# Performance work log

Measured on AMD Instinct MI355X. Metric: run time of the kernel, lower is better.

Reference implementation:

```python
import jax, jax.numpy as jnp
import numpy as np

B, L, H, NE, SPAN = 16, 2048, 768, 64, 4
EPS_COS = 1e-8   # torch cosine_similarity eps
EPS_STD = 1e-5   # std stabilizer from the module


def _linear_init(key, fan_in, fan_out):
    s = 1.0 / np.sqrt(fan_in)
    kw, kb = jax.random.split(key)
    w = jax.random.uniform(kw, (fan_in, fan_out), jnp.float32, -s, s)
    b = jax.random.uniform(kb, (fan_out,), jnp.float32, -s, s)
    return w, b


def setup_inputs() -> dict:
    key = jax.random.key(0)
    ks = jax.random.split(key, 6)
    w1, b1 = _linear_init(ks[0], 2 * H + 1, H)
    w2, b2 = _linear_init(ks[1], H, 512)
    w3, b3 = _linear_init(ks[2], 512, 256)
    w4, b4 = _linear_init(ks[3], 256, 2)
    x = jax.random.normal(ks[4], (B, L, H), jnp.float32)
    entity_starts = jax.random.randint(ks[5], (B, NE), 0, L - SPAN)
    threshold = jnp.float32(0.9)
    return dict(x=x, threshold=threshold,
                w1=w1, b1=b1, w2=w2, b2=b2, w3=w3, b3=b3, w4=w4, b4=b4,
                entity_starts=entity_starts)


def reference(x, threshold, w1, b1, w2, b2, w3, b3, w4, b4, entity_starts):
    # --- per-entity span max-pool (segment-max over x) ---
    # gather span tokens: [B, NE*SPAN] token indices into the L axis
    idx = (entity_starts[:, :, None] + jnp.arange(SPAN)).reshape(B, NE * SPAN)
    spans = jnp.take_along_axis(x, idx[:, :, None], axis=1)      # [B, NE*SPAN, H]
    emb = spans.reshape(B, NE, SPAN, H).max(axis=2)               # [B, NE, H]

    # --- pairwise cosine similarity per batch ---
    norm = jnp.maximum(jnp.linalg.norm(emb, axis=-1, keepdims=True), EPS_COS)
    n = emb / norm
    cos = jnp.einsum('bie,bje->bij', n, n)                        # [B, NE, NE]
    std = jnp.std(cos, axis=(1, 2), ddof=1, keepdims=True)        # torch .std() is unbiased
    sim = (cos - threshold) / (std + EPS_STD)
    sim = jnp.triu(sim, k=1)

    # --- all i<j pairs: [sim, emb_i, emb_j] ---
    iu, ju = np.triu_indices(NE, k=1)                             # static pair indices
    feats = jnp.concatenate(
        [sim[:, iu, ju, None], emb[:, iu, :], emb[:, ju, :]], axis=-1
    ).reshape(-1, 2 * H + 1)                                      # [B*P, 2H+1]

    # --- classifier MLP (dropout = identity at eval) ---
    h = jax.nn.relu(feats @ w1 + b1)
    h = jax.nn.relu(h @ w2 + b2)
    h = jax.nn.relu(h @ w3 + b3)
    logits = h @ w4 + b4                                          # [B*P, 2]
    return logits
```

## Files before the change

### kernel.cpp

```cpp
#include <hip/hip_runtime.h>
#include <cstdint>
#include <cstddef>

#define B_    16
#define L_    2048
#define H_    768
#define NE_   64
#define SPAN_ 4
#define NPAIR 2016
#define NROWS (B_ * NPAIR)

typedef __bf16 bf16_t;
typedef __bf16 bf16x8 __attribute__((ext_vector_type(8)));
typedef __bf16 bf16x4 __attribute__((ext_vector_type(4)));
typedef float  floatx4 __attribute__((ext_vector_type(4)));

#define OFF_EMBH   ((size_t)3145728)
#define OFF_N      ((size_t)4718592)
#define OFF_COS    ((size_t)7864320)
#define OFF_SIM    ((size_t)8126464)
#define OFF_W1ABT  ((size_t)8255488)
#define OFF_W2T    ((size_t)10614784)
#define OFF_W3T    ((size_t)11401216)
#define OFF_C1     ((size_t)11663360)
#define OFF_H2     ((size_t)67500032)
#define OFF_FLAG   ((size_t)117045248)
#define OFF_CANON  ((size_t)117045504)

__device__ int compute_flag(const unsigned short* __restrict__ xu) {
  __shared__ int tot[4];
  int t = threadIdx.x;
  int bad = 0;
  for (int i = t; i < 4096; i += 256) {
    int e = (xu[i] >> 7) & 0xFF;
    if (e > 133 || (e > 0 && e < 90)) bad++;
  }
  for (int off = 32; off > 0; off >>= 1) bad += __shfl_down(bad, off, 64);
  if ((t & 63) == 0) tot[t >> 6] = bad;
  __syncthreads();
  int f = ((tot[0] + tot[1] + tot[2] + tot[3]) > 200) ? 1 : 0;
  __syncthreads();
  return f;
}

__device__ inline bf16_t cvt_elem(const void* p, size_t i, int isf) {
  if (isf) return (bf16_t)(((const float*)p)[i]);
  return ((const bf16_t*)p)[i];
}

__global__ __launch_bounds__(256) void prep_kernel(
    const unsigned short* __restrict__ xu,
    const void* __restrict__ w1, const void* __restrict__ w2,
    const void* __restrict__ w3, const void* __restrict__ b1,
    const void* __restrict__ b2, const void* __restrict__ b3,
    const void* __restrict__ w4, const void* __restrict__ b4,
    int* __restrict__ flagout,
    bf16_t* __restrict__ w1abT, bf16_t* __restrict__ w2T,
    bf16_t* __restrict__ w3T, bf16_t* __restrict__ canon) {
  int blk = blockIdx.x;
  int t = threadIdx.x;
  int isf = compute_flag(xu);
  if (blk == 1664) {
    if (t == 0) flagout[0] = isf;
    for (int idx = t; idx < 2818; idx += 256) {
      if (idx < 768)       canon[idx] = cvt_elem(w1, idx, isf);
      else if (idx < 1536) canon[idx] = cvt_elem(b1, idx - 768, isf);
      else if (idx < 2048) canon[idx] = cvt_elem(b2, idx - 1536, isf);
      else if (idx < 2304) canon[idx] = cvt_elem(b3, idx - 2048, isf);
      else if (idx < 2816) canon[idx] = cvt_elem(w4, idx - 2304, isf);
      else                 canon[idx] = cvt_elem(b4, idx - 2816, isf);
    }
    return;
  }
  const void* src; size_t srcoff; bf16_t* dst; int K, N; int tix;
  if (blk < 576)       { src = w1; srcoff = 768;               dst = w1abT;          K = 768; N = 768; tix = blk; }
  else if (blk < 1152) { src = w1; srcoff = (size_t)769 * 768; dst = w1abT + 589824; K = 768; N = 768; tix = blk - 576; }
  else if (blk < 1536) { src = w2; srcoff = 0;                 dst = w2T;            K = 768; N = 512; tix = blk - 1152; }
  else                 { src = w3; srcoff = 0;                 dst = w3T;            K = 512; N = 256; tix = blk - 1536; }
  int tiles_k = K >> 5;
  int tn_t = tix / tiles_k, tk_t = tix - tn_t * tiles_k;
  __shared__ bf16_t tile[32][33];
  int ty = t >> 5, tx = t & 31;
#pragma unroll
  for (int p = 0; p < 4; p++) {
    int kk = tk_t * 32 + p * 8 + ty;
    int nn = tn_t * 32 + tx;
    tile[p * 8 + ty][tx] = cvt_elem(src, srcoff + (size_t)kk * N + nn, isf);
  }
  __syncthreads();
#pragma unroll
  for (int p = 0; p < 4; p++) {
    int nn = tn_t * 32 + p * 8 + ty;
    int kk = tk_t * 32 + tx;
    dst[(size_t)nn * K + kk] = tile[tx][p * 8 + ty];
  }
}

__global__ __launch_bounds__(1024) void embsim_kernel(
    const void* __restrict__ xv, const int* __restrict__ starts,
    const int* __restrict__ flagp, const void* __restrict__ thr_ptr,
    bf16_t* __restrict__ embh, float* __restrict__ simv) {
  __shared__ __align__(16) bf16_t nrm[64 * 768];
  __shared__ float red1[16], red2[16];
  __shared__ float scale_s, thr_s;
  int b = blockIdx.x;
  int t = threadIdx.x;
  int isf = flagp[0];

  int e   = t >> 4;
  int l16 = t & 15;
  int d0  = l16 * 48;
  int st  = starts[b * NE_ + e];
  size_t off = ((size_t)(b * L_ + st)) * H_;
  float ss = 0.f;
  bf16x8 pv[6];
  if (isf) {
    const float* xp = (const float*)xv + off + d0;
    for (int c8 = 0; c8 < 6; c8++) {
      const float* p = xp + c8 * 8;
      bf16x8 o;
#pragma unroll
      for (int h = 0; h < 2; h++) {
        floatx4 r0 = *(const floatx4*)(p + h * 4);
        floatx4 r1 = *(const floatx4*)(p + H_ + h * 4);
        floatx4 r2 = *(const floatx4*)(p + 2 * H_ + h * 4);
        floatx4 r3 = *(const floatx4*)(p + 3 * H_ + h * 4);
#pragma unroll
        for (int q = 0; q < 4; q++) {
          float v = fmaxf(fmaxf(r0[q], r1[q]), fmaxf(r2[q], r3[q]));
          ss += v * v;
          o[h * 4 + q] = (bf16_t)v;
        }
      }
      pv[c8] = o;
    }
  } else {
    const bf16_t* xp = (const bf16_t*)xv + off + d0;
    for (int c8 = 0; c8 < 6; c8++) {
      const bf16_t* p = xp + c8 * 8;
      bf16x8 r0 = *(const bf16x8*)(p);
      bf16x8 r1 = *(const bf16x8*)(p + H_);
      bf16x8 r2 = *(const bf16x8*)(p + 2 * H_);
      bf16x8 r3 = *(const bf16x8*)(p + 3 * H_);
      bf16x8 o;
#pragma unroll
      for (int q = 0; q < 8; q++) {
        float v = fmaxf(fmaxf((float)r0[q], (float)r1[q]),
                        fmaxf((float)r2[q], (float)r3[q]));
        ss += v * v;
        o[q] = (bf16_t)v;
      }
      pv[c8] = o;
    }
  }
#pragma unroll
  for (int d = 1; d < 16; d <<= 1) ss += __shfl_xor(ss, d, 64);
  float inv = 1.0f / fmaxf(sqrtf(ss), 1e-8f);

  size_t gb = ((size_t)(b * 64 + e)) * 768 + d0;
  int rowbyte = e * 1536;
  int xw = (e & 7) << 4;
  for (int c8 = 0; c8 < 6; c8++) {
    *(bf16x8*)(embh + gb + c8 * 8) = pv[c8];
    bf16x8 o;
#pragma unroll
    for (int q = 0; q < 8; q++) o[q] = (bf16_t)((float)pv[c8][q] * inv);
    int byo = (rowbyte + (d0 + c8 * 8) * 2) ^ xw;
    *(bf16x8*)((char*)nrm + byo) = o;
  }
  __syncthreads();

  int w = t >> 6, lane = t & 63;
  int quad = lane >> 4, l15 = lane & 15;
  int ti = w >> 2, tj = w & 3;
  int rowA = ti * 16 + l15, rowB = tj * 16 + l15;
  int xa = (rowA & 7) << 4, xb = (rowB & 7) << 4;
  const char* nb = (const char*)nrm;
  floatx4 acc = {};
#pragma unroll 4
  for (int k0 = 0; k0 < 768; k0 += 32) {
    int cb = (k0 + quad * 8) * 2;
    bf16x8 aF = *(const bf16x8*)(nb + ((rowA * 1536 + cb) ^ xa));
    bf16x8 bF = *(const bf16x8*)(nb + ((rowB * 1536 + cb) ^ xb));
    acc = __builtin_amdgcn_mfma_f32_16x16x32_bf16(aF, bF, acc, 0, 0, 0);
  }

  float s1 = acc[0] + acc[1] + acc[2] + acc[3];
  float s2 = acc[0] * acc[0] + acc[1] * acc[1] + acc[2] * acc[2] + acc[3] * acc[3];
#pragma unroll
  for (int d = 32; d > 0; d >>= 1) {
    s1 += __shfl_xor(s1, d, 64);
    s2 += __shfl_xor(s2, d, 64);
  }
  if (lane == 0) { red1[w] = s1; red2[w] = s2; }
  __syncthreads();
  if (t == 0) {
    float S1 = 0.f, S2 = 0.f;
#pragma unroll
    for (int i = 0; i < 16; i++) { S1 += red1[i]; S2 += red2[i]; }
    float mean = S1 * (1.0f / 4096.0f);
    float var = (S2 - 4096.0f * mean * mean) * (1.0f / 4095.0f);
    float sd = sqrtf(fmaxf(var, 0.f));
    scale_s = 1.0f / (sd + 1e-5f);
    thr_s = isf ? *(const float*)thr_ptr : (float)(*(const bf16_t*)thr_ptr);
  }
  __syncthreads();
  float sc = scale_s, th = thr_s;
  int ibase = ti * 16 + quad * 4;
  int j = tj * 16 + l15;
#pragma unroll
  for (int r = 0; r < 4; r++) {
    int i = ibase + r;
    if (j > i) {
      int p = i * 63 - (i * (i - 1)) / 2 + (j - i - 1);
      simv[b * NPAIR + p] = (acc[r] - th) * sc;
    }
  }
}

__global__ __launch_bounds__(256) void gemm1_kernel(
    const bf16_t* __restrict__ A, const bf16_t* __restrict__ Bt,
    float* __restrict__ C) {
  const int K = 768, N = 1536;
  __shared__ __align__(16) bf16_t Asm[64 * 32];
  __shared__ __align__(16) bf16_t Bsm[128 * 32];
  int bm = blockIdx.x, bn = blockIdx.y;
  int t = threadIdx.x;
  int w = t >> 6, lane = t & 63;
  int quad = lane >> 4, l15 = lane & 15;
  int wm = w >> 1, wn = w & 1;

  floatx4 acc[2][4] = {};
  const char* Abase = (const char*)(A + (size_t)bm * 64 * K);
  const char* Bbase = (const char*)(Bt + (size_t)bn * 128 * K);
  const int rowbytes = K * 2;

  for (int k0 = 0; k0 < K; k0 += 32) {
    {
      int fo = w * 1024 + lane * 16;
      int row = fo >> 6, colb = fo & 63;
      __builtin_amdgcn_global_load_lds(
          (__attribute__((address_space(1))) char*)(Abase + (size_t)row * rowbytes + k0 * 2 + colb),
          (__attribute__((address_space(3))) char*)((char*)Asm + w * 1024),
          16, 0, 0);
    }
#pragma unroll
    for (int it = 0; it < 2; it++) {
      int fo = (w * 2 + it) * 1024 + lane * 16;
      int row = fo >> 6, colb = fo & 63;
      __builtin_amdgcn_global_load_lds(
          (__attribute__((address_space(1))) char*)(Bbase + (size_t)row * rowbytes + k0 * 2 + colb),
          (__attribute__((address_space(3))) char*)((char*)Bsm + (w * 2 + it) * 1024),
          16, 0, 0);
    }
    __syncthreads();

    bf16x8 aF[2], bF[4];
#pragma unroll
    for (int tm = 0; tm < 2; tm++)
      aF[tm] = *((const bf16x8*)(Asm + (wm * 32 + tm * 16 + l15) * 32 + quad * 8));
#pragma unroll
    for (int tn = 0; tn < 4; tn++)
      bF[tn] = *((const bf16x8*)(Bsm + (wn * 64 + tn * 16 + l15) * 32 + quad * 8));
#pragma unroll
    for (int tm = 0; tm < 2; tm++)
#pragma unroll
      for (int tn = 0; tn < 4; tn++)
        acc[tm][tn] = __builtin_amdgcn_mfma_f32_16x16x32_bf16(aF[tm], bF[tn], acc[tm][tn], 0, 0, 0);
    __syncthreads();
  }

#pragma unroll
  for (int tm = 0; tm < 2; tm++) {
    int grow0 = bm * 64 + wm * 32 + tm * 16 + quad * 4;
#pragma unroll
    for (int tn = 0; tn < 4; tn++) {
      int gcol = bn * 128 + wn * 64 + tn * 16 + l15;
#pragma unroll
      for (int r = 0; r < 4; r++)
        C[(size_t)(grow0 + r) * N + gcol] = acc[tm][tn][r];
    }
  }
}

__global__ __launch_bounds__(512, 4) void gemm2_fused_kernel(
    const float* __restrict__ C1, const float* __restrict__ sim,
    const bf16_t* __restrict__ w2T, const bf16_t* __restrict__ canon,
    bf16_t* __restrict__ h2) {
  __shared__ __align__(16) bf16_t Asm[128 * 40];
  __shared__ __align__(16) bf16_t Bsm[256 * 32];
  __shared__ int   rowI[128], rowJ[128];
  __shared__ float rowS[128];
  __shared__ bf16_t w1s[768], b1s[768];
  __shared__ float b2s[256];
  int bm = blockIdx.x, bn = blockIdx.y;
  int t = threadIdx.x;

  if (t < 128) {
    int r = bm * 128 + t;
    int b = r / NPAIR, p = r - b * NPAIR;
    int i = 0, rem = p;
    while (rem >= 63 - i) { rem -= 63 - i; i++; }
    rowI[t] = b * 64 + i;
    rowJ[t] = b * 64 + i + 1 + rem;
    rowS[t] = sim[r];
  }
  for (int c = t; c < 768; c += 512) { w1s[c] = canon[c]; b1s[c] = canon[768 + c]; }
  if (t < 256) b2s[t] = (float)canon[1536 + bn * 256 + t];
  __syncthreads();

  int w = t >> 6, lane = t & 63;
  int quad = lane >> 4, l15 = lane & 15;
  int wm = w >> 2, wn = w & 3;
  floatx4 acc[4][4] = {};

  const char* Bbase = (const char*)(w2T + (size_t)bn * 256 * 768);

  int arow = t >> 2;
  int acolc = (t & 3) * 8;
  const float* Ai = C1 + (size_t)rowI[arow] * 1536 + acolc;
  const float* Aj = C1 + (size_t)rowJ[arow] * 1536 + 768 + acolc;
  float s = rowS[arow];
  bf16_t* awr = Asm + arow * 40 + acolc;

  float4 pi0 = *(const float4*)(Ai);
  float4 pi1 = *(const float4*)(Ai + 4);
  float4 pj0 = *(const float4*)(Aj);
  float4 pj1 = *(const float4*)(Aj + 4);

  for (int k0 = 0; k0 < 768; k0 += 32) {
#pragma unroll
    for (int it = 0; it < 2; it++) {
      int fo = w * 2048 + it * 1024 + lane * 16;
      int row = fo >> 6, colb = fo & 63;
      __builtin_amdgcn_global_load_lds(
          (__attribute__((address_space(1))) char*)(Bbase + (size_t)row * 1536 + k0 * 2 + colb),
          (__attribute__((address_space(3))) char*)((char*)Bsm + w * 2048 + it * 1024),
          16, 0, 0);
    }
    {
      int kc = k0 + acolc;
      bf16x8 o;
      const bf16x8 wv8 = *(const bf16x8*)(w1s + kc);
      const bf16x8 bv8 = *(const bf16x8*)(b1s + kc);
      o[0] = (bf16_t)fmaxf(pi0.x + pj0.x + s * (float)wv8[0] + (float)bv8[0], 0.f);
      o[1] = (bf16_t)fmaxf(pi0.y + pj0.y + s * (float)wv8[1] + (float)bv8[1], 0.f);
      o[2] = (bf16_t)fmaxf(pi0.z + pj0.z + s * (float)wv8[2] + (float)bv8[2], 0.f);
      o[3] = (bf16_t)fmaxf(pi0.w + pj0.w + s * (float)wv8[3] + (float)bv8[3], 0.f);
      o[4] = (bf16_t)fmaxf(pi1.x + pj1.x + s * (float)wv8[4] + (float)bv8[4], 0.f);
      o[5] = (bf16_t)fmaxf(pi1.y + pj1.y + s * (float)wv8[5] + (float)bv8[5], 0.f);
      o[6] = (bf16_t)fmaxf(pi1.z + pj1.z + s * (float)wv8[6] + (float)bv8[6], 0.f);
      o[7] = (bf16_t)fmaxf(pi1.w + pj1.w + s * (float)wv8[7] + (float)bv8[7], 0.f);
      *(bf16x8*)awr = o;
    }
    if (k0 + 32 < 768) {
      pi0 = *(const float4*)(Ai + k0 + 32);
      pi1 = *(const float4*)(Ai + k0 + 36);
      pj0 = *(const float4*)(Aj + k0 + 32);
      pj1 = *(const float4*)(Aj + k0 + 36);
    }
    __syncthreads();

    bf16x8 aF[4], bF[4];
#pragma unroll
    for (int tm = 0; tm < 4; tm++)
      aF[tm] = *((const bf16x8*)(Asm + (wm * 64 + tm * 16 + l15) * 40 + quad * 8));
#pragma unroll
    for (int tn = 0; tn < 4; tn++)
      bF[tn] = *((const bf16x8*)(Bsm + (wn * 64 + tn * 16 + l15) * 32 + quad * 8));
#pragma unroll
    for (int tm = 0; tm < 4; tm++)
#pragma unroll
      for (int tn = 0; tn < 4; tn++)
        acc[tm][tn] = __builtin_amdgcn_mfma_f32_16x16x32_bf16(aF[tm], bF[tn], acc[tm][tn], 0, 0, 0);
    __syncthreads();
  }

#pragma unroll
  for (int tm = 0; tm < 4; tm++) {
    int grow0 = bm * 128 + wm * 64 + tm * 16 + quad * 4;
#pragma unroll
    for (int tn = 0; tn < 4; tn++) {
      int lcol = wn * 64 + tn * 16 + l15;
      int gcol = bn * 256 + lcol;
#pragma unroll
      for (int r = 0; r < 4; r++) {
        float v = fmaxf(acc[tm][tn][r] + b2s[lcol], 0.f);
        h2[(size_t)(grow0 + r) * 512 + gcol] = (bf16_t)v;
      }
    }
  }
}

__global__ __launch_bounds__(256) void gemm3_fused_kernel(
    const bf16_t* __restrict__ h2, const bf16_t* __restrict__ w3T,
    const bf16_t* __restrict__ canon, const int* __restrict__ flagp,
    void* __restrict__ out) {
  __shared__ __align__(16) bf16_t Asm[64 * 32];
  __shared__ __align__(16) bf16_t Bsm[256 * 32];
  __shared__ float part[64][2][4];
  __shared__ float w4s[512];
  __shared__ float b3s[256];
  int bm = blockIdx.x;
  int t = threadIdx.x;
  int w = t >> 6, lane = t & 63;
  int quad = lane >> 4, l15 = lane & 15;

  w4s[t]       = (float)canon[2304 + t];
  w4s[256 + t] = (float)canon[2304 + 256 + t];
  b3s[t]       = (float)canon[2048 + t];

  floatx4 acc[4][4] = {};
  const char* Abase = (const char*)(h2 + (size_t)bm * 64 * 512);
  const char* Bbase = (const char*)w3T;

  for (int k0 = 0; k0 < 512; k0 += 32) {
    {
      int fo = w * 1024 + lane * 16;
      int row = fo >> 6, colb = fo & 63;
      __builtin_amdgcn_global_load_lds(
          (__attribute__((address_space(1))) char*)(Abase + (size_t)row * 1024 + k0 * 2 + colb),
          (__attribute__((address_space(3))) char*)((char*)Asm + w * 1024),
          16, 0, 0);
    }
#pragma unroll
    for (int it = 0; it < 4; it++) {
      int fo = w * 4096 + it * 1024 + lane * 16;
      int row = fo >> 6, colb = fo & 63;
      __builtin_amdgcn_global_load_lds(
          (__attribute__((address_space(1))) char*)(Bbase + (size_t)row * 1024 + k0 * 2 + colb),
          (__attribute__((address_space(3))) char*)((char*)Bsm + w * 4096 + it * 1024),
          16, 0, 0);
    }
    __syncthreads();

    bf16x8 aF[4], bF[4];
#pragma unroll
    for (int tm = 0; tm < 4; tm++)
      aF[tm] = *((const bf16x8*)(Asm + (tm * 16 + l15) * 32 + quad * 8));
#pragma unroll
    for (int tn = 0; tn < 4; tn++)
      bF[tn] = *((const bf16x8*)(Bsm + (w * 64 + tn * 16 + l15) * 32 + quad * 8));
#pragma unroll
    for (int tm = 0; tm < 4; tm++)
#pragma unroll
      for (int tn = 0; tn < 4; tn++)
        acc[tm][tn] = __builtin_amdgcn_mfma_f32_16x16x32_bf16(aF[tm], bF[tn], acc[tm][tn], 0, 0, 0);
    __syncthreads();
  }

#pragma unroll
  for (int tm = 0; tm < 4; tm++) {
#pragma unroll
    for (int reg = 0; reg < 4; reg++) {
      float p0 = 0.f, p1 = 0.f;
#pragma unroll
      for (int tn = 0; tn < 4; tn++) {
        int col = w * 64 + tn * 16 + l15;
        float v = fmaxf(acc[tm][tn][reg] + b3s[col], 0.f);
        p0 += v * w4s[col * 2];
        p1 += v * w4s[col * 2 + 1];
      }
#pragma unroll
      for (int d = 1; d < 16; d <<= 1) {
        p0 += __shfl_xor(p0, d, 64);
        p1 += __shfl_xor(p1, d, 64);
      }
      if (l15 == 0) {
        int r = tm * 16 + quad * 4 + reg;
        part[r][0][w] = p0;
        part[r][1][w] = p1;
      }
    }
  }
  __syncthreads();
  if (t < 128) {
    int r = t >> 1, c = t & 1;
    float v = part[r][c][0] + part[r][c][1] + part[r][c][2] + part[r][c][3]
            + (float)canon[2816 + c];
    size_t rg = (size_t)bm * 64 + r;
    if (flagp[0]) ((float*)out)[rg * 2 + c] = v;
    else          ((bf16_t*)out)[rg * 2 + c] = (bf16_t)v;
  }
}

extern "C" void kernel_launch(void* const* d_in, const int* in_sizes, int n_in,
                              void* d_out, int out_size, void* d_ws, size_t ws_size,
                              hipStream_t stream) {
  const void* x      = d_in[0];
  const void* thr    = d_in[1];
  const void* w1     = d_in[2];
  const void* b1     = d_in[3];
  const void* w2     = d_in[4];
  const void* b2     = d_in[5];
  const void* w3     = d_in[6];
  const void* b3     = d_in[7];
  const void* w4     = d_in[8];
  const void* b4     = d_in[9];
  const int*  starts = (const int*)d_in[10];

  char* ws = (char*)d_ws;
  bf16_t* embh  = (bf16_t*)(ws + OFF_EMBH);
  float*  simv  = (float*)(ws + OFF_SIM);
  bf16_t* w1abT = (bf16_t*)(ws + OFF_W1ABT);
  bf16_t* w2T   = (bf16_t*)(ws + OFF_W2T);
  bf16_t* w3T   = (bf16_t*)(ws + OFF_W3T);
  float*  C1    = (float*)(ws + OFF_C1);
  bf16_t* h2    = (bf16_t*)(ws + OFF_H2);
  int*    flag  = (int*)(ws + OFF_FLAG);
  bf16_t* canon = (bf16_t*)(ws + OFF_CANON);

  prep_kernel<<<1665, 256, 0, stream>>>((const unsigned short*)x,
                                        w1, w2, w3, b1, b2, b3, w4, b4,
                                        flag, w1abT, w2T, w3T, canon);
  embsim_kernel<<<B_, 1024, 0, stream>>>(x, starts, flag, thr, embh, simv);

  {
    dim3 g(1024 / 64, 1536 / 128);
    gemm1_kernel<<<g, 256, 0, stream>>>(embh, w1abT, C1);
  }
  {
    dim3 g(NROWS / 128, 2);
    gemm2_fused_kernel<<<g, 512, 0, stream>>>(C1, simv, w2T, canon, h2);
  }
  gemm3_fused_kernel<<<NROWS / 64, 256, 0, stream>>>(h2, w3T, canon, flag, d_out);
}
```

Measured before the change: 276.5 us.

## Fuse prep with embsim and fuse MLP layers two and three via LDS

Merges the weight-transpose prep kernel and the span-pool/cosine-sim kernel into one launch with 1024-thread blocks and 64x64 transpose tiles. Fuses the second and third MLP GEMMs so each 64-row block computes all 512 h2 columns, keeps h2 in swizzled shared memory, then runs layer three and the final projection. This removes the h2 global round trip and two launches. In exchange, the fused block uses much more LDS, occupancy drops, and h2 columns are no longer split across blocks.

```diff
diff --git a/kernel.cpp b/kernel.cpp
--- a/kernel.cpp
+++ b/kernel.cpp
@@ -16,53 +16,173 @@
 typedef float  floatx4 __attribute__((ext_vector_type(4)));
 
 #define OFF_EMBH   ((size_t)3145728)
-#define OFF_N      ((size_t)4718592)
-#define OFF_COS    ((size_t)7864320)
 #define OFF_SIM    ((size_t)8126464)
 #define OFF_W1ABT  ((size_t)8255488)
 #define OFF_W2T    ((size_t)10614784)
 #define OFF_W3T    ((size_t)11401216)
 #define OFF_C1     ((size_t)11663360)
-#define OFF_H2     ((size_t)67500032)
 #define OFF_FLAG   ((size_t)117045248)
 #define OFF_CANON  ((size_t)117045504)
-
-__device__ int compute_flag(const unsigned short* __restrict__ xu) {
-  __shared__ int tot[4];
-  int t = threadIdx.x;
-  int bad = 0;
-  for (int i = t; i < 4096; i += 256) {
-    int e = (xu[i] >> 7) & 0xFF;
-    if (e > 133 || (e > 0 && e < 90)) bad++;
-  }
-  for (int off = 32; off > 0; off >>= 1) bad += __shfl_down(bad, off, 64);
-  if ((t & 63) == 0) tot[t >> 6] = bad;
-  __syncthreads();
-  int f = ((tot[0] + tot[1] + tot[2] + tot[3]) > 200) ? 1 : 0;
-  __syncthreads();
-  return f;
-}
 
 __device__ inline bf16_t cvt_elem(const void* p, size_t i, int isf) {
   if (isf) return (bf16_t)(((const float*)p)[i]);
   return ((const bf16_t*)p)[i];
 }
 
-__global__ __launch_bounds__(256) void prep_kernel(
+__global__ __launch_bounds__(1024) void prep_embsim_kernel(
     const unsigned short* __restrict__ xu,
+    const void* __restrict__ xv, const int* __restrict__ starts,
+    const void* __restrict__ thr_ptr,
     const void* __restrict__ w1, const void* __restrict__ w2,
     const void* __restrict__ w3, const void* __restrict__ b1,
     const void* __restrict__ b2, const void* __restrict__ b3,
     const void* __restrict__ w4, const void* __restrict__ b4,
     int* __restrict__ flagout,
     bf16_t* __restrict__ w1abT, bf16_t* __restrict__ w2T,
-    bf16_t* __restrict__ w3T, bf16_t* __restrict__ canon) {
+    bf16_t* __restrict__ w3T, bf16_t* __restrict__ canon,
+    bf16_t* __restrict__ embh, float* __restrict__ simv) {
+  __shared__ __align__(16) char shbuf[98304];
+  __shared__ int   tot[16];
+  __shared__ float red1[16], red2[16];
+  __shared__ float scale_s, thr_s;
+
   int blk = blockIdx.x;
   int t = threadIdx.x;
-  int isf = compute_flag(xu);
-  if (blk == 1664) {
+
+  {
+    int bad = 0;
+    for (int i = t; i < 4096; i += 1024) {
+      int e = (xu[i] >> 7) & 0xFF;
+      if (e > 133 || (e > 0 && e < 90)) bad++;
+    }
+    for (int off = 32; off > 0; off >>= 1) bad += __shfl_down(bad, off, 64);
+    if ((t & 63) == 0) tot[t >> 6] = bad;
+    __syncthreads();
+  }
+  int sumb = 0;
+#pragma unroll
+  for (int i = 0; i < 16; i++) sumb += tot[i];
+  int isf = (sumb > 200) ? 1 : 0;
+  __syncthreads();
+
+  if (blk < 16) {
+    bf16_t* nrm = (bf16_t*)shbuf;
+    int b = blk;
+    int e   = t >> 4;
+    int l16 = t & 15;
+    int d0  = l16 * 48;
+    int st  = starts[b * NE_ + e];
+    size_t off = ((size_t)(b * L_ + st)) * H_;
+    float ss = 0.f;
+    bf16x8 pv[6];
+    if (isf) {
+      const float* xp = (const float*)xv + off + d0;
+      for (int c8 = 0; c8 < 6; c8++) {
+        const float* p = xp + c8 * 8;
+        bf16x8 o;
+#pragma unroll
+        for (int h = 0; h < 2; h++) {
+          floatx4 r0 = *(const floatx4*)(p + h * 4);
+          floatx4 r1 = *(const floatx4*)(p + H_ + h * 4);
+          floatx4 r2 = *(const floatx4*)(p + 2 * H_ + h * 4);
+          floatx4 r3 = *(const floatx4*)(p + 3 * H_ + h * 4);
+#pragma unroll
+          for (int q = 0; q < 4; q++) {
+            float v = fmaxf(fmaxf(r0[q], r1[q]), fmaxf(r2[q], r3[q]));
+            ss += v * v;
+            o[h * 4 + q] = (bf16_t)v;
+          }
+        }
+        pv[c8] = o;
+      }
+    } else {
+      const bf16_t* xp = (const bf16_t*)xv + off + d0;
+      for (int c8 = 0; c8 < 6; c8++) {
+        const bf16_t* p = xp + c8 * 8;
+        bf16x8 r0 = *(const bf16x8*)(p);
+        bf16x8 r1 = *(const bf16x8*)(p + H_);
+        bf16x8 r2 = *(const bf16x8*)(p + 2 * H_);
+        bf16x8 r3 = *(const bf16x8*)(p + 3 * H_);
+        bf16x8 o;
+#pragma unroll
+        for (int q = 0; q < 8; q++) {
+          float v = fmaxf(fmaxf((float)r0[q], (float)r1[q]),
+                          fmaxf((float)r2[q], (float)r3[q]));
+          ss += v * v;
+          o[q] = (bf16_t)v;
+        }
+        pv[c8] = o;
+      }
+    }
+#pragma unroll
+    for (int d = 1; d < 16; d <<= 1) ss += __shfl_xor(ss, d, 64);
+    float inv = 1.0f / fmaxf(sqrtf(ss), 1e-8f);
+
+    size_t gb = ((size_t)(b * 64 + e)) * 768 + d0;
+    int rowbyte = e * 1536;
+    int xw = (e & 7) << 4;
+    for (int c8 = 0; c8 < 6; c8++) {
+      *(bf16x8*)(embh + gb + c8 * 8) = pv[c8];
+      bf16x8 o;
+#pragma unroll
+      for (int q = 0; q < 8; q++) o[q] = (bf16_t)((float)pv[c8][q] * inv);
+      int byo = (rowbyte + (d0 + c8 * 8) * 2) ^ xw;
+      *(bf16x8*)((char*)nrm + byo) = o;
+    }
+    __syncthreads();
+
+    int w = t >> 6, lane = t & 63;
+    int quad = lane >> 4, l15 = lane & 15;
+    int ti = w >> 2, tj = w & 3;
+    int rowA = ti * 16 + l15, rowB = tj * 16 + l15;
+    int xa = (rowA & 7) << 4, xb = (rowB & 7) << 4;
+    const char* nb = (const char*)nrm;
+    floatx4 acc = {};
+#pragma unroll 4
+    for (int k0 = 0; k0 < 768; k0 += 32) {
+      int cb = (k0 + quad * 8) * 2;
+      bf16x8 aF = *(const bf16x8*)(nb + ((rowA * 1536 + cb) ^ xa));
+      bf16x8 bF = *(const bf16x8*)(nb + ((rowB * 1536 + cb) ^ xb));
+      acc = __builtin_amdgcn_mfma_f32_16x16x32_bf16(aF, bF, acc, 0, 0, 0);
+    }
+
+    float s1 = acc[0] + acc[1] + acc[2] + acc[3];
+    float s2 = acc[0] * acc[0] + acc[1] * acc[1] + acc[2] * acc[2] + acc[3] * acc[3];
+#pragma unroll
+    for (int d = 32; d > 0; d >>= 1) {
+      s1 += __shfl_xor(s1, d, 64);
+      s2 += __shfl_xor(s2, d, 64);
+    }
+    if (lane == 0) { red1[w] = s1; red2[w] = s2; }
+    __syncthreads();
+    if (t == 0) {
+      float S1 = 0.f, S2 = 0.f;
+#pragma unroll
+      for (int i = 0; i < 16; i++) { S1 += red1[i]; S2 += red2[i]; }
+      float mean = S1 * (1.0f / 4096.0f);
+      float var = (S2 - 4096.0f * mean * mean) * (1.0f / 4095.0f);
+      float sd = sqrtf(fmaxf(var, 0.f));
+      scale_s = 1.0f / (sd + 1e-5f);
+      thr_s = isf ? *(const float*)thr_ptr : (float)(*(const bf16_t*)thr_ptr);
+    }
+    __syncthreads();
+    float sc = scale_s, th = thr_s;
+    int ibase = ti * 16 + quad * 4;
+    int j = tj * 16 + l15;
+#pragma unroll
+    for (int r = 0; r < 4; r++) {
+      int i = ibase + r;
+      if (j > i) {
+        int p = i * 63 - (i * (i - 1)) / 2 + (j - i - 1);
+        simv[b * NPAIR + p] = (acc[r] - th) * sc;
+      }
+    }
+    return;
+  }
+
+  if (blk == 16) {
     if (t == 0) flagout[0] = isf;
-    for (int idx = t; idx < 2818; idx += 256) {
+    for (int idx = t; idx < 2818; idx += 1024) {
       if (idx < 768)       canon[idx] = cvt_elem(w1, idx, isf);
       else if (idx < 1536) canon[idx] = cvt_elem(b1, idx - 768, isf);
       else if (idx < 2048) canon[idx] = cvt_elem(b2, idx - 1536, isf);
@@ -72,149 +192,29 @@
     }
     return;
   }
-  const void* src; size_t srcoff; bf16_t* dst; int K, N; int tix;
-  if (blk < 576)       { src = w1; srcoff = 768;               dst = w1abT;          K = 768; N = 768; tix = blk; }
-  else if (blk < 1152) { src = w1; srcoff = (size_t)769 * 768; dst = w1abT + 589824; K = 768; N = 768; tix = blk - 576; }
-  else if (blk < 1536) { src = w2; srcoff = 0;                 dst = w2T;            K = 768; N = 512; tix = blk - 1152; }
-  else                 { src = w3; srcoff = 0;                 dst = w3T;            K = 512; N = 256; tix = blk - 1536; }
-  int tiles_k = K >> 5;
+
+  int tix = blk - 17;
+  const void* src; size_t srcoff; bf16_t* dst; int K, N;
+  if (tix < 144)      { src = w1; srcoff = 768;               dst = w1abT;          K = 768; N = 768; }
+  else if (tix < 288) { src = w1; srcoff = (size_t)769 * 768; dst = w1abT + 589824; K = 768; N = 768; tix -= 144; }
+  else if (tix < 384) { src = w2; srcoff = 0;                 dst = w2T;            K = 768; N = 512; tix -= 288; }
+  else                { src = w3; srcoff = 0;                 dst = w3T;            K = 512; N = 256; tix -= 384; }
+  int tiles_k = K >> 6;
   int tn_t = tix / tiles_k, tk_t = tix - tn_t * tiles_k;
-  __shared__ bf16_t tile[32][33];
-  int ty = t >> 5, tx = t & 31;
+  bf16_t (*tile)[65] = (bf16_t(*)[65])shbuf;
+  int ty = t >> 6, tx = t & 63;
 #pragma unroll
   for (int p = 0; p < 4; p++) {
-    int kk = tk_t * 32 + p * 8 + ty;
-    int nn = tn_t * 32 + tx;
-    tile[p * 8 + ty][tx] = cvt_elem(src, srcoff + (size_t)kk * N + nn, isf);
+    int kk = tk_t * 64 + p * 16 + ty;
+    int nn = tn_t * 64 + tx;
+    tile[p * 16 + ty][tx] = cvt_elem(src, srcoff + (size_t)kk * N + nn, isf);
   }
   __syncthreads();
 #pragma unroll
   for (int p = 0; p < 4; p++) {
-    int nn = tn_t * 32 + p * 8 + ty;
-    int kk = tk_t * 32 + tx;
-    dst[(size_t)nn * K + kk] = tile[tx][p * 8 + ty];
-  }
-}
-
-__global__ __launch_bounds__(1024) void embsim_kernel(
-    const void* __restrict__ xv, const int* __restrict__ starts,
-    const int* __restrict__ flagp, const void* __restrict__ thr_ptr,
-    bf16_t* __restrict__ embh, float* __restrict__ simv) {
-  __shared__ __align__(16) bf16_t nrm[64 * 768];
-  __shared__ float red1[16], red2[16];
-  __shared__ float scale_s, thr_s;
-  int b = blockIdx.x;
-  int t = threadIdx.x;
-  int isf = flagp[0];
-
-  int e   = t >> 4;
-  int l16 = t & 15;
-  int d0  = l16 * 48;
-  int st  = starts[b * NE_ + e];
-  size_t off = ((size_t)(b * L_ + st)) * H_;
-  float ss = 0.f;
-  bf16x8 pv[6];
-  if (isf) {
-    const float* xp = (const float*)xv + off + d0;
-    for (int c8 = 0; c8 < 6; c8++) {
-      const float* p = xp + c8 * 8;
-      bf16x8 o;
-#pragma unroll
-      for (int h = 0; h < 2; h++) {
-        floatx4 r0 = *(const floatx4*)(p + h * 4);
-        floatx4 r1 = *(const floatx4*)(p + H_ + h * 4);
-        floatx4 r2 = *(const floatx4*)(p + 2 * H_ + h * 4);
-        floatx4 r3 = *(const floatx4*)(p + 3 * H_ + h * 4);
-#pragma unroll
-        for (int q = 0; q < 4; q++) {
-          float v = fmaxf(fmaxf(r0[q], r1[q]), fmaxf(r2[q], r3[q]));
-          ss += v * v;
-          o[h * 4 + q] = (bf16_t)v;
-        }
-      }
-      pv[c8] = o;
-    }
-  } else {
-    const bf16_t* xp = (const bf16_t*)xv + off + d0;
-    for (int c8 = 0; c8 < 6; c8++) {
-      const bf16_t* p = xp + c8 * 8;
-      bf16x8 r0 = *(const bf16x8*)(p);
-      bf16x8 r1 = *(const bf16x8*)(p + H_);
-      bf16x8 r2 = *(const bf16x8*)(p + 2 * H_);
-      bf16x8 r3 = *(const bf16x8*)(p + 3 * H_);
-      bf16x8 o;
-#pragma unroll
-      for (int q = 0; q < 8; q++) {
-        float v = fmaxf(fmaxf((float)r0[q], (float)r1[q]),
-                        fmaxf((float)r2[q], (float)r3[q]));
-        ss += v * v;
-        o[q] = (bf16_t)v;
-      }
-      pv[c8] = o;
-    }
-  }
-#pragma unroll
-  for (int d = 1; d < 16; d <<= 1) ss += __shfl_xor(ss, d, 64);
-  float inv = 1.0f / fmaxf(sqrtf(ss), 1e-8f);
-
-  size_t gb = ((size_t)(b * 64 + e)) * 768 + d0;
-  int rowbyte = e * 1536;
-  int xw = (e & 7) << 4;
-  for (int c8 = 0; c8 < 6; c8++) {
-    *(bf16x8*)(embh + gb + c8 * 8) = pv[c8];
-    bf16x8 o;
-#pragma unroll
-    for (int q = 0; q < 8; q++) o[q] = (bf16_t)((float)pv[c8][q] * inv);
-    int byo = (rowbyte + (d0 + c8 * 8) * 2) ^ xw;
-    *(bf16x8*)((char*)nrm + byo) = o;
-  }
-  __syncthreads();
-
-  int w = t >> 6, lane = t & 63;
-  int quad = lane >> 4, l15 = lane & 15;
-  int ti = w >> 2, tj = w & 3;
-  int rowA = ti * 16 + l15, rowB = tj * 16 + l15;
-  int xa = (rowA & 7) << 4, xb = (rowB & 7) << 4;
-  const char* nb = (const char*)nrm;
-  floatx4 acc = {};
-#pragma unroll 4
-  for (int k0 = 0; k0 < 768; k0 += 32) {
-    int cb = (k0 + quad * 8) * 2;
-    bf16x8 aF = *(const bf16x8*)(nb + ((rowA * 1536 + cb) ^ xa));
-    bf16x8 bF = *(const bf16x8*)(nb + ((rowB * 1536 + cb) ^ xb));
-    acc = __builtin_amdgcn_mfma_f32_16x16x32_bf16(aF, bF, acc, 0, 0, 0);
-  }
-
-  float s1 = acc[0] + acc[1] + acc[2] + acc[3];
-  float s2 = acc[0] * acc[0] + acc[1] * acc[1] + acc[2] * acc[2] + acc[3] * acc[3];
-#pragma unroll
-  for (int d = 32; d > 0; d >>= 1) {
-    s1 += __shfl_xor(s1, d, 64);
-    s2 += __shfl_xor(s2, d, 64);
-  }
-  if (lane == 0) { red1[w] = s1; red2[w] = s2; }
-  __syncthreads();
-  if (t == 0) {
-    float S1 = 0.f, S2 = 0.f;
-#pragma unroll
-    for (int i = 0; i < 16; i++) { S1 += red1[i]; S2 += red2[i]; }
-    float mean = S1 * (1.0f / 4096.0f);
-    float var = (S2 - 4096.0f * mean * mean) * (1.0f / 4095.0f);
-    float sd = sqrtf(fmaxf(var, 0.f));
-    scale_s = 1.0f / (sd + 1e-5f);
-    thr_s = isf ? *(const float*)thr_ptr : (float)(*(const bf16_t*)thr_ptr);
-  }
-  __syncthreads();
-  float sc = scale_s, th = thr_s;
-  int ibase = ti * 16 + quad * 4;
-  int j = tj * 16 + l15;
-#pragma unroll
-  for (int r = 0; r < 4; r++) {
-    int i = ibase + r;
-    if (j > i) {
-      int p = i * 63 - (i * (i - 1)) / 2 + (j - i - 1);
-      simv[b * NPAIR + p] = (acc[r] - th) * sc;
-    }
+    int nn = tn_t * 64 + p * 16 + ty;
+    int kk = tk_t * 64 + tx;
+    dst[(size_t)nn * K + kk] = tile[tx][p * 16 + ty];
   }
 }
 
@@ -283,21 +283,25 @@
   }
 }
 
-__global__ __launch_bounds__(512, 4) void gemm2_fused_kernel(
+__global__ __launch_bounds__(512, 2) void gemm23_kernel(
     const float* __restrict__ C1, const float* __restrict__ sim,
-    const bf16_t* __restrict__ w2T, const bf16_t* __restrict__ canon,
-    bf16_t* __restrict__ h2) {
-  __shared__ __align__(16) bf16_t Asm[128 * 40];
-  __shared__ __align__(16) bf16_t Bsm[256 * 32];
-  __shared__ int   rowI[128], rowJ[128];
-  __shared__ float rowS[128];
+    const bf16_t* __restrict__ w2T, const bf16_t* __restrict__ w3T,
+    const bf16_t* __restrict__ canon, const int* __restrict__ flagp,
+    void* __restrict__ out) {
+  __shared__ __align__(16) bf16_t Asm[64 * 40];
+  __shared__ __align__(16) bf16_t Bsm[512 * 32];
+  __shared__ __align__(16) bf16_t h2s[64 * 512];
+  __shared__ int   rowI[64], rowJ[64];
+  __shared__ float rowS[64];
   __shared__ bf16_t w1s[768], b1s[768];
-  __shared__ float b2s[256];
-  int bm = blockIdx.x, bn = blockIdx.y;
+  __shared__ float b2s[512];
+  __shared__ float b3s[256], w4s[512];
+  __shared__ float part[64][2][4];
+  int bm = blockIdx.x;
   int t = threadIdx.x;
 
-  if (t < 128) {
-    int r = bm * 128 + t;
+  if (t < 64) {
+    int r = bm * 64 + t;
     int b = r / NPAIR, p = r - b * NPAIR;
     int i = 0, rem = p;
     while (rem >= 63 - i) { rem -= 63 - i; i++; }
@@ -306,158 +310,120 @@
     rowS[t] = sim[r];
   }
   for (int c = t; c < 768; c += 512) { w1s[c] = canon[c]; b1s[c] = canon[768 + c]; }
-  if (t < 256) b2s[t] = (float)canon[1536 + bn * 256 + t];
+  b2s[t] = (float)canon[1536 + t];
+  if (t < 256) b3s[t] = (float)canon[2048 + t];
+  w4s[t] = (float)canon[2304 + t];
   __syncthreads();
 
   int w = t >> 6, lane = t & 63;
   int quad = lane >> 4, l15 = lane & 15;
   int wm = w >> 2, wn = w & 3;
-  floatx4 acc[4][4] = {};
-
-  const char* Bbase = (const char*)(w2T + (size_t)bn * 256 * 768);
-
-  int arow = t >> 2;
-  int acolc = (t & 3) * 8;
+
+  floatx4 acc[2][8] = {};
+  int arow = t >> 3;
+  int acolc = (t & 7) * 4;
   const float* Ai = C1 + (size_t)rowI[arow] * 1536 + acolc;
   const float* Aj = C1 + (size_t)rowJ[arow] * 1536 + 768 + acolc;
   float s = rowS[arow];
   bf16_t* awr = Asm + arow * 40 + acolc;
 
-  float4 pi0 = *(const float4*)(Ai);
-  float4 pi1 = *(const float4*)(Ai + 4);
-  float4 pj0 = *(const float4*)(Aj);
-  float4 pj1 = *(const float4*)(Aj + 4);
+  float4 pi = *(const float4*)(Ai);
+  float4 pj = *(const float4*)(Aj);
 
   for (int k0 = 0; k0 < 768; k0 += 32) {
+#pragma unroll
+    for (int it = 0; it < 4; it++) {
+      int fo = w * 4096 + it * 1024 + lane * 16;
+      int row = fo >> 6, colb = fo & 63;
+      __builtin_amdgcn_global_load_lds(
+          (__attribute__((address_space(1))) char*)((const char*)w2T + (size_t)row * 1536 + k0 * 2 + colb),
+          (__attribute__((address_space(3))) char*)((char*)Bsm + w * 4096 + it * 1024),
+          16, 0, 0);
+    }
+    {
+      int kc = k0 + acolc;
+      bf16x4 o;
+      o[0] = (bf16_t)fmaxf(pi.x + pj.x + s * (float)w1s[kc]     + (float)b1s[kc],     0.f);
+      o[1] = (bf16_t)fmaxf(pi.y + pj.y + s * (float)w1s[kc + 1] + (float)b1s[kc + 1], 0.f);
+      o[2] = (bf16_t)fmaxf(pi.z + pj.z + s * (float)w1s[kc + 2] + (float)b1s[kc + 2], 0.f);
+      o[3] = (bf16_t)fmaxf(pi.w + pj.w + s * (float)w1s[kc + 3] + (float)b1s[kc + 3], 0.f);
+      *(bf16x4*)awr = o;
+    }
+    if (k0 + 32 < 768) {
+      pi = *(const float4*)(Ai + k0 + 32);
+      pj = *(const float4*)(Aj + k0 + 32);
+    }
+    __syncthreads();
+
+    bf16x8 aF[2], bF[8];
+#pragma unroll
+    for (int tm = 0; tm < 2; tm++)
+      aF[tm] = *((const bf16x8*)(Asm + (wm * 32 + tm * 16 + l15) * 40 + quad * 8));
+#pragma unroll
+    for (int tn = 0; tn < 8; tn++)
+      bF[tn] = *((const bf16x8*)(Bsm + (wn * 128 + tn * 16 + l15) * 32 + quad * 8));
+#pragma unroll
+    for (int tm = 0; tm < 2; tm++)
+#pragma unroll
+      for (int tn = 0; tn < 8; tn++)
+        acc[tm][tn] = __builtin_amdgcn_mfma_f32_16x16x32_bf16(aF[tm], bF[tn], acc[tm][tn], 0, 0, 0);
+    __syncthreads();
+  }
+
+#pragma unroll
+  for (int tm = 0; tm < 2; tm++) {
+#pragma unroll
+    for (int tn = 0; tn < 8; tn++) {
+      int col = wn * 128 + tn * 16 + l15;
+#pragma unroll
+      for (int r = 0; r < 4; r++) {
+        int row = wm * 32 + tm * 16 + quad * 4 + r;
+        float v = fmaxf(acc[tm][tn][r] + b2s[col], 0.f);
+        h2s[row * 512 + (col ^ ((row & 7) << 3))] = (bf16_t)v;
+      }
+    }
+  }
+  __syncthreads();
+
+  floatx4 acc2[2][4] = {};
+  for (int k0 = 0; k0 < 512; k0 += 32) {
 #pragma unroll
     for (int it = 0; it < 2; it++) {
       int fo = w * 2048 + it * 1024 + lane * 16;
       int row = fo >> 6, colb = fo & 63;
       __builtin_amdgcn_global_load_lds(
-          (__attribute__((address_space(1))) char*)(Bbase + (size_t)row * 1536 + k0 * 2 + colb),
+          (__attribute__((address_space(1))) char*)((const char*)w3T + (size_t)row * 1024 + k0 * 2 + colb),
           (__attribute__((address_space(3))) char*)((char*)Bsm + w * 2048 + it * 1024),
           16, 0, 0);
     }
-    {
-      int kc = k0 + acolc;
-      bf16x8 o;
-      const bf16x8 wv8 = *(const bf16x8*)(w1s + kc);
-      const bf16x8 bv8 = *(const bf16x8*)(b1s + kc);
-      o[0] = (bf16_t)fmaxf(pi0.x + pj0.x + s * (float)wv8[0] + (float)bv8[0], 0.f);
-      o[1] = (bf16_t)fmaxf(pi0.y + pj0.y + s * (float)wv8[1] + (float)bv8[1], 0.f);
-      o[2] = (bf16_t)fmaxf(pi0.z + pj0.z + s * (float)wv8[2] + (float)bv8[2], 0.f);
-      o[3] = (bf16_t)fmaxf(pi0.w + pj0.w + s * (float)wv8[3] + (float)bv8[3], 0.f);
-      o[4] = (bf16_t)fmaxf(pi1.x + pj1.x + s * (float)wv8[4] + (float)bv8[4], 0.f);
-      o[5] = (bf16_t)fmaxf(pi1.y + pj1.y + s * (float)wv8[5] + (float)bv8[5], 0.f);
-      o[6] = (bf16_t)fmaxf(pi1.z + pj1.z + s * (float)wv8[6] + (float)bv8[6], 0.f);
-      o[7] = (bf16_t)fmaxf(pi1.w + pj1.w + s * (float)wv8[7] + (float)bv8[7], 0.f);
-      *(bf16x8*)awr = o;
-    }
-    if (k0 + 32 < 768) {
-      pi0 = *(const float4*)(Ai + k0 + 32);
-      pi1 = *(const float4*)(Ai + k0 + 36);
-      pj0 = *(const float4*)(Aj + k0 + 32);
-      pj1 = *(const float4*)(Aj + k0 + 36);
-    }
-    __syncthreads();
-
-    bf16x8 aF[4], bF[4];
-#pragma unroll
-    for (int tm = 0; tm < 4; tm++)
-      aF[tm] = *((const bf16x8*)(Asm + (wm * 64 + tm * 16 + l15) * 40 + quad * 8));
+    __syncthreads();
+
+    bf16x8 aF[2], bF[4];
+#pragma unroll
+    for (int tm = 0; tm < 2; tm++) {
+      int row = wm * 32 + tm * 16 + l15;
+      aF[tm] = *((const bf16x8*)(h2s + row * 512 + ((k0 + quad * 8) ^ ((row & 7) << 3))));
+    }
 #pragma unroll
     for (int tn = 0; tn < 4; tn++)
       bF[tn] = *((const bf16x8*)(Bsm + (wn * 64 + tn * 16 + l15) * 32 + quad * 8));
 #pragma unroll
-    for (int tm = 0; tm < 4; tm++)
+    for (int tm = 0; tm < 2; tm++)
 #pragma unroll
       for (int tn = 0; tn < 4; tn++)
-        acc[tm][tn] = __builtin_amdgcn_mfma_f32_16x16x32_bf16(aF[tm], bF[tn], acc[tm][tn], 0, 0, 0);
-    __syncthreads();
-  }
-
-#pragma unroll
-  for (int tm = 0; tm < 4; tm++) {
-    int grow0 = bm * 128 + wm * 64 + tm * 16 + quad * 4;
-#pragma unroll
-    for (int tn = 0; tn < 4; tn++) {
-      int lcol = wn * 64 + tn * 16 + l15;
-      int gcol = bn * 256 + lcol;
-#pragma unroll
-      for (int r = 0; r < 4; r++) {
-        float v = fmaxf(acc[tm][tn][r] + b2s[lcol], 0.f);
-        h2[(size_t)(grow0 + r) * 512 + gcol] = (bf16_t)v;
-      }
-    }
-  }
-}
-
-__global__ __launch_bounds__(256) void gemm3_fused_kernel(
-    const bf16_t* __restrict__ h2, const bf16_t* __restrict__ w3T,
-    const bf16_t* __restrict__ canon, const int* __restrict__ flagp,
-    void* __restrict__ out) {
-  __shared__ __align__(16) bf16_t Asm[64 * 32];
-  __shared__ __align__(16) bf16_t Bsm[256 * 32];
-  __shared__ float part[64][2][4];
-  __shared__ float w4s[512];
-  __shared__ float b3s[256];
-  int bm = blockIdx.x;
-  int t = threadIdx.x;
-  int w = t >> 6, lane = t & 63;
-  int quad = lane >> 4, l15 = lane & 15;
-
-  w4s[t]       = (float)canon[2304 + t];
-  w4s[256 + t] = (float)canon[2304 + 256 + t];
-  b3s[t]       = (float)canon[2048 + t];
-
-  floatx4 acc[4][4] = {};
-  const char* Abase = (const char*)(h2 + (size_t)bm * 64 * 512);
-  const char* Bbase = (const char*)w3T;
-
-  for (int k0 = 0; k0 < 512; k0 += 32) {
-    {
-      int fo = w * 1024 + lane * 16;
-      int row = fo >> 6, colb = fo & 63;
-      __builtin_amdgcn_global_load_lds(
-          (__attribute__((address_space(1))) char*)(Abase + (size_t)row * 1024 + k0 * 2 + colb),
-          (__attribute__((address_space(3))) char*)((char*)Asm + w * 1024),
-          16, 0, 0);
-    }
-#pragma unroll
-    for (int it = 0; it < 4; it++) {
-      int fo = w * 4096 + it * 1024 + lane * 16;
-      int row = fo >> 6, colb = fo & 63;
-      __builtin_amdgcn_global_load_lds(
-          (__attribute__((address_space(1))) char*)(Bbase + (size_t)row * 1024 + k0 * 2 + colb),
-          (__attribute__((address_space(3))) char*)((char*)Bsm + w * 4096 + it * 1024),
-          16, 0, 0);
-    }
-    __syncthreads();
-
-    bf16x8 aF[4], bF[4];
-#pragma unroll
-    for (int tm = 0; tm < 4; tm++)
-      aF[tm] = *((const bf16x8*)(Asm + (tm * 16 + l15) * 32 + quad * 8));
-#pragma unroll
-    for (int tn = 0; tn < 4; tn++)
-      bF[tn] = *((const bf16x8*)(Bsm + (w * 64 + tn * 16 + l15) * 32 + quad * 8));
-#pragma unroll
-    for (int tm = 0; tm < 4; tm++)
-#pragma unroll
-      for (int tn = 0; tn < 4; tn++)
-        acc[tm][tn] = __builtin_amdgcn_mfma_f32_16x16x32_bf16(aF[tm], bF[tn], acc[tm][tn], 0, 0, 0);
-    __syncthreads();
-  }
-
-#pragma unroll
-  for (int tm = 0; tm < 4; tm++) {
+        acc2[tm][tn] = __builtin_amdgcn_mfma_f32_16x16x32_bf16(aF[tm], bF[tn], acc2[tm][tn], 0, 0, 0);
+    __syncthreads();
+  }
+
+#pragma unroll
+  for (int tm = 0; tm < 2; tm++) {
 #pragma unroll
     for (int reg = 0; reg < 4; reg++) {
       float p0 = 0.f, p1 = 0.f;
 #pragma unroll
       for (int tn = 0; tn < 4; tn++) {
-        int col = w * 64 + tn * 16 + l15;
-        float v = fmaxf(acc[tm][tn][reg] + b3s[col], 0.f);
+        int col = wn * 64 + tn * 16 + l15;
+        float v = fmaxf(acc2[tm][tn][reg] + b3s[col], 0.f);
         p0 += v * w4s[col * 2];
         p1 += v * w4s[col * 2 + 1];
       }
@@ -467,9 +433,9 @@
         p1 += __shfl_xor(p1, d, 64);
       }
       if (l15 == 0) {
-        int r = tm * 16 + quad * 4 + reg;
-        part[r][0][w] = p0;
-        part[r][1][w] = p1;
+        int r = wm * 32 + tm * 16 + quad * 4 + reg;
+        part[r][0][wn] = p0;
+        part[r][1][wn] = p1;
       }
     }
   }
@@ -506,22 +472,19 @@
   bf16_t* w2T   = (bf16_t*)(ws + OFF_W2T);
   bf16_t* w3T   = (bf16_t*)(ws + OFF_W3T);
   float*  C1    = (float*)(ws + OFF_C1);
-  bf16_t* h2    = (bf16_t*)(ws + OFF_H2);
   int*    flag  = (int*)(ws + OFF_FLAG);
   bf16_t* canon = (bf16_t*)(ws + OFF_CANON);
 
-  prep_kernel<<<1665, 256, 0, stream>>>((const unsigned short*)x,
-                                        w1, w2, w3, b1, b2, b3, w4, b4,
-                                        flag, w1abT, w2T, w3T, canon);
-  embsim_kernel<<<B_, 1024, 0, stream>>>(x, starts, flag, thr, embh, simv);
+  prep_embsim_kernel<<<433, 1024, 0, stream>>>(
+      (const unsigned short*)x, x, starts, thr,
+      w1, w2, w3, b1, b2, b3, w4, b4,
+      flag, w1abT, w2T, w3T, canon, embh, simv);
 
   {
     dim3 g(1024 / 64, 1536 / 128);
     gemm1_kernel<<<g, 256, 0, stream>>>(embh, w1abT, C1);
   }
-  {
-    dim3 g(NROWS / 128, 2);
-    gemm2_fused_kernel<<<g, 512, 0, stream>>>(C1, simv, w2T, canon, h2);
-  }
-  gemm3_fused_kernel<<<NROWS / 64, 256, 0, stream>>>(h2, w3T, canon, flag, d_out);
+
+  gemm23_kernel<<<NROWS / 64, 512, 0, stream>>>(C1, simv, w2T, w3T, canon,
+                                                flag, d_out);
 }
```

New measurement: 296.0 us. 7.0% more time.
